# Performance work log

Measured on AMD Instinct MI355X. Metric: run time of the kernel, lower is better.

## Reference

```python
import jax, jax.numpy as jnp
import numpy as np

N_HEAD = 16


def setup_inputs() -> dict:
    key = jax.random.key(0)
    k1, k2, k3 = jax.random.split(key, 3)
    B, T, C = 2, 2048, 1024
    x = jax.random.normal(k1, (B, T, C), dtype=jnp.float32)
    # stored as [in, out] so projection is x @ w (equiv. to torch Linear with W=[out,in])
    w_attn = jax.random.normal(k2, (C, 3 * C), dtype=jnp.float32) * 0.02
    w_proj = jax.random.normal(k3, (C, C), dtype=jnp.float32) * 0.02
    return {"x": x, "w_attn": w_attn, "w_proj": w_proj}


def reference(x, w_attn, w_proj):
    B, T, C = x.shape
    H = N_HEAD
    D = C // H
    qkv = x @ w_attn                                  # [B,T,3C]
    q, k, v = jnp.split(qkv, 3, axis=-1)
    q = q.reshape(B, T, H, D).transpose(0, 2, 1, 3)   # [B,H,T,D]
    k = k.reshape(B, T, H, D).transpose(0, 2, 1, 3)
    v = v.reshape(B, T, H, D).transpose(0, 2, 1, 3)
    scale = 1.0 / jnp.sqrt(jnp.asarray(D, dtype=x.dtype))
    att = jnp.einsum("bhqd,bhkd->bhqk", q, k) * scale  # [B,H,T,T]
    causal = jnp.tril(jnp.ones((T, T), dtype=bool))
    att = jnp.where(causal[None, None], att, jnp.finfo(att.dtype).min)
    att = jax.nn.softmax(att, axis=-1)                 # dropout p=0 (eval)
    y = jnp.einsum("bhqk,bhkd->bhqd", att, v)          # [B,H,T,D]
    y = y.transpose(0, 2, 1, 3).reshape(B, T, C)
    return y @ w_proj
```

## Files before the change

kernel.cpp:

```cpp
#include <hip/hip_runtime.h>

using u16 = unsigned short;
using u32 = unsigned int;

typedef __attribute__((ext_vector_type(8))) short s16x8;
typedef __attribute__((ext_vector_type(4))) short s16x4;
typedef __attribute__((ext_vector_type(8))) __bf16 bf16x8;
typedef __attribute__((ext_vector_type(4))) float f32x4;

static __device__ __forceinline__ u16 f2bf(float f) {
  u32 u = __builtin_bit_cast(u32, f);
  u32 r = u + 0x7FFFu + ((u >> 16) & 1u);
  return (u16)(r >> 16);
}

static __device__ __forceinline__ f32x4 mfma16(s16x8 a, s16x8 b, f32x4 c) {
  return __builtin_amdgcn_mfma_f32_16x16x32_bf16(
      __builtin_bit_cast(bf16x8, a), __builtin_bit_cast(bf16x8, b), c, 0, 0, 0);
}

#define GLOAD_LDS16(gp, lp)                                                    \
  __builtin_amdgcn_global_load_lds(                                            \
      (const __attribute__((address_space(1))) void*)(gp),                     \
      (__attribute__((address_space(3))) void*)(lp), 16, 0, 0)

__global__ __launch_bounds__(256) void k_cvt(const float* __restrict__ in,
                                             u16* __restrict__ out, int n) {
  int i = (blockIdx.x * 256 + threadIdx.x) * 8;
  if (i >= n) return;
  const float4 v0 = *(const float4*)(in + i);
  const float4 v1 = *(const float4*)(in + i + 4);
  s16x8 o;
  o[0] = f2bf(v0.x); o[1] = f2bf(v0.y); o[2] = f2bf(v0.z); o[3] = f2bf(v0.w);
  o[4] = f2bf(v1.x); o[5] = f2bf(v1.y); o[6] = f2bf(v1.z); o[7] = f2bf(v1.w);
  *(s16x8*)(out + i) = o;
}

__global__ __launch_bounds__(256) void k_transpose_cvt(const float* __restrict__ src,
                                                       u16* __restrict__ dst,
                                                       int K, int N) {
  __shared__ float tile[64][65];
  const int n0 = blockIdx.x * 64, k0 = blockIdx.y * 64;
  const int c = threadIdx.x & 63, r4 = threadIdx.x >> 6;
#pragma unroll
  for (int i = 0; i < 16; ++i) {
    int r = (i << 2) + r4;
    tile[r][c] = src[(k0 + r) * N + n0 + c];
  }
  __syncthreads();
#pragma unroll
  for (int i = 0; i < 16; ++i) {
    int r = (i << 2) + r4;
    dst[(n0 + r) * K + k0 + c] = f2bf(tile[c][r]);
  }
}

template <int MODE>
__global__ __launch_bounds__(256) void k_gemm(
    const u16* __restrict__ A, const u16* __restrict__ BT,
    u16* __restrict__ qg, u16* __restrict__ kg, u16* __restrict__ vtg,
    float* __restrict__ cout, int M, int N, int K) {
  __shared__ __align__(16) u16 As[128 * 32];
  __shared__ __align__(16) u16 Bs[128 * 32];
  __shared__ __align__(16) u16 Ct[(MODE == 0) ? (128 * 132) : 8];
  const int t = threadIdx.x;
  const int lane = t & 63;
  const int w = t >> 6, wr = w >> 1, wc = w & 1;
  const int lrow = lane & 15, lkg = lane >> 4;
  const int m0 = blockIdx.y * 128, n0 = blockIdx.x * 128;

  const int ch1 = t + 256;
  const int ra0 = t >> 2, ca0 = (t & 3) << 3;
  const int ra1 = ch1 >> 2, ca1 = (ch1 & 3) << 3;
  const u16* gA0 = A + (m0 + ra0) * K + ca0;
  const u16* gA1 = A + (m0 + ra1) * K + ca1;
  const u16* gB0 = BT + (n0 + ra0) * K + ca0;
  const u16* gB1 = BT + (n0 + ra1) * K + ca1;
  u16* lA0 = &As[t * 8];
  u16* lA1 = &As[ch1 * 8];
  u16* lB0 = &Bs[t * 8];
  u16* lB1 = &Bs[ch1 * 8];

  f32x4 acc[4][4];
#pragma unroll
  for (int m = 0; m < 4; ++m)
#pragma unroll
    for (int n = 0; n < 4; ++n) acc[m][n] = (f32x4){0.f, 0.f, 0.f, 0.f};

  for (int k0 = 0; k0 < K; k0 += 32) {
    GLOAD_LDS16(gA0 + k0, lA0);
    GLOAD_LDS16(gA1 + k0, lA1);
    GLOAD_LDS16(gB0 + k0, lB0);
    GLOAD_LDS16(gB1 + k0, lB1);
    __syncthreads();
    s16x8 af[4], bfr[4];
#pragma unroll
    for (int m = 0; m < 4; ++m)
      af[m] = *(const s16x8*)&As[(wr * 64 + m * 16 + lrow) * 32 + lkg * 8];
#pragma unroll
    for (int n = 0; n < 4; ++n)
      bfr[n] = *(const s16x8*)&Bs[(wc * 64 + n * 16 + lrow) * 32 + lkg * 8];
#pragma unroll
    for (int m = 0; m < 4; ++m)
#pragma unroll
      for (int n = 0; n < 4; ++n) acc[m][n] = mfma16(af[m], bfr[n], acc[m][n]);
    __syncthreads();
  }

  if (MODE == 0) {
    const int part = n0 >> 10;
    const int b = m0 >> 11;
    const int tt0 = m0 & 2047;
    if (part < 2) {
#pragma unroll
      for (int m = 0; m < 4; ++m)
#pragma unroll
        for (int n = 0; n < 4; ++n)
#pragma unroll
          for (int r = 0; r < 4; ++r) {
            const int tl = wr * 64 + m * 16 + lkg * 4 + r;
            const int rem = (n0 & 1023) + wc * 64 + n * 16 + lrow;
            const int h = rem >> 6, d = rem & 63;
            const int bh = b * 16 + h;
            const float v = acc[m][n][r];
            if (part == 0)
              qg[(bh * 2048 + tt0 + tl) * 64 + d] = f2bf(v * 0.18033688f);
            else
              kg[(bh * 2048 + tt0 + tl) * 64 + d] = f2bf(v);
          }
    } else {
#pragma unroll
      for (int m = 0; m < 4; ++m)
#pragma unroll
        for (int n = 0; n < 4; ++n) {
          const int cl2 = wc * 64 + n * 16 + lrow;
          const int tl = wr * 64 + m * 16 + lkg * 4;
          s16x4 pk;
#pragma unroll
          for (int r = 0; r < 4; ++r) pk[r] = f2bf(acc[m][n][r]);
          *(s16x4*)&Ct[cl2 * 132 + tl] = pk;
        }
      __syncthreads();
      const long vrow0 = (long)b * 1024 + (n0 & 1023);
      const int cl = t >> 1;
      const int ch = (t & 1) << 6;
      const u16* csrc = &Ct[cl * 132 + ch];
      u16* vdst = vtg + (vrow0 + cl) * 2048 + tt0 + ch;
#pragma unroll
      for (int j = 0; j < 8; ++j) {
        const s16x4 a4 = *(const s16x4*)&csrc[j * 8];
        const s16x4 b4 = *(const s16x4*)&csrc[j * 8 + 4];
        s16x8 v8;
        v8[0] = a4[0]; v8[1] = a4[1]; v8[2] = a4[2]; v8[3] = a4[3];
        v8[4] = b4[0]; v8[5] = b4[1]; v8[6] = b4[2]; v8[7] = b4[3];
        *(s16x8*)&vdst[j * 8] = v8;
      }
    }
  } else {
#pragma unroll
    for (int m = 0; m < 4; ++m)
#pragma unroll
      for (int n = 0; n < 4; ++n)
#pragma unroll
        for (int r = 0; r < 4; ++r) {
          const int rg = m0 + wr * 64 + m * 16 + lkg * 4 + r;
          const int cg = n0 + wc * 64 + n * 16 + lrow;
          cout[rg * N + cg] = acc[m][n][r];
        }
  }
}

__global__ __launch_bounds__(256) void k_attn(const u16* __restrict__ qg,
                                              const u16* __restrict__ kg,
                                              const u16* __restrict__ vtg,
                                              u16* __restrict__ yb) {
  __shared__ __align__(16) u16 Ks[2][64 * 64];
  __shared__ __align__(16) u16 Vs[2][64 * 64];
  __shared__ __align__(16) u16 Ps[4][32 * 72];
  const int t = threadIdx.x;
  const int lane = t & 63, w = t >> 6;
  const int lrow = lane & 15, lkg = lane >> 4;
  const int bx = blockIdx.x, by = blockIdx.y;
  const int qs = (by & 16) ? (15 - bx) : bx;
  const int bh = by;
  const int qw0 = qs * 128 + w * 32;
  const int hb = bh & 15, bb = bh >> 4;
  const int sw = lrow & 7;
  const f32x4 z4 = {0.f, 0.f, 0.f, 0.f};

  const u16* kbase = kg + ((long)bh << 11) * 64;
  const u16* vbase = vtg + ((long)bh << 6) * 2048;

  const int srow = lane >> 3;
  const int sxor8 = ((lane & 7) ^ srow) << 3;

  s16x8 aq[2][2];
#pragma unroll
  for (int m = 0; m < 2; ++m)
#pragma unroll
    for (int kk = 0; kk < 2; ++kk)
      aq[m][kk] = *(const s16x8*)&qg[((bh << 11) + qw0 + m * 16 + lrow) * 64 +
                                     kk * 32 + lkg * 8];

  f32x4 o[2][4];
  float mst[2], lst[2];
#pragma unroll
  for (int m = 0; m < 2; ++m) {
#pragma unroll
    for (int d = 0; d < 4; ++d) o[m][d] = z4;
    mst[m] = -3e38f;
    lst[m] = 0.f;
  }

  const int nt = 2 * qs + 2;

#define STAGE(BUF, TT)                                                         \
  {                                                                            \
    const int kv0s = (TT) << 6;                                                \
    _Pragma("unroll") for (int i = 0; i < 2; ++i) {                            \
      const int rr = ((i * 4 + w) << 3) + srow;                                \
      const int dst = (((i * 4 + w) << 6) + lane) << 3;                        \
      GLOAD_LDS16(kbase + ((kv0s + rr) << 6) + sxor8, &Ks[BUF][dst]);          \
      GLOAD_LDS16(vbase + ((long)rr << 11) + kv0s + sxor8, &Vs[BUF][dst]);     \
    }                                                                          \
  }

  STAGE(0, 0);
  int buf = 0;
  for (int tt = 0; tt < nt; ++tt) {
    const int kv0 = tt << 6;
    if (tt + 1 < nt) {
      STAGE(buf ^ 1, tt + 1);
      asm volatile("s_waitcnt vmcnt(4)" ::: "memory");
    } else {
      asm volatile("s_waitcnt vmcnt(0)" ::: "memory");
    }
    __builtin_amdgcn_s_barrier();
    __builtin_amdgcn_sched_barrier(0);

    if (kv0 < qw0 + 32) {
      f32x4 s[2][4];
      __builtin_amdgcn_s_setprio(1);
#pragma unroll
      for (int c = 0; c < 4; ++c) {
        const int krow = c * 16 + lrow;
        s16x8 bk0 = *(const s16x8*)&Ks[buf][krow * 64 + ((lkg ^ sw) << 3)];
        s16x8 bk1 = *(const s16x8*)&Ks[buf][krow * 64 + (((4 + lkg) ^ sw) << 3)];
#pragma unroll
        for (int m = 0; m < 2; ++m)
          s[m][c] = mfma16(bk1, aq[m][1], mfma16(bk0, aq[m][0], z4));
      }
      __builtin_amdgcn_s_setprio(0);

      if (kv0 + 64 > qw0) {
#pragma unroll
        for (int m = 0; m < 2; ++m) {
          const int qrow = qw0 + m * 16 + lrow;
#pragma unroll
          for (int c = 0; c < 4; ++c) {
            const int kvb = kv0 + c * 16 + lkg * 4;
#pragma unroll
            for (int r = 0; r < 4; ++r)
              if (kvb + r > qrow) s[m][c][r] = -3e38f;
          }
        }
      }

      u16* PW = Ps[w];
#pragma unroll
      for (int m = 0; m < 2; ++m) {
        float lm = s[m][0][0];
#pragma unroll
        for (int c = 0; c < 4; ++c)
#pragma unroll
          for (int r = 0; r < 4; ++r) lm = fmaxf(lm, s[m][c][r]);
        lm = fmaxf(lm, __shfl_xor(lm, 16));
        lm = fmaxf(lm, __shfl_xor(lm, 32));
        const float mn = fmaxf(mst[m], lm);
        const float alm = exp2f(mst[m] - mn);
        mst[m] = mn;
        float ss = 0.f;
#pragma unroll
        for (int c = 0; c < 4; ++c)
#pragma unroll
          for (int r = 0; r < 4; ++r) {
            const float p = exp2f(s[m][c][r] - mn);
            s[m][c][r] = p;
            ss += p;
          }
        ss += __shfl_xor(ss, 16);
        ss += __shfl_xor(ss, 32);
        lst[m] = alm * lst[m] + ss;
#pragma unroll
        for (int d = 0; d < 4; ++d) o[m][d] *= alm;
#pragma unroll
        for (int c = 0; c < 4; ++c) {
          s16x4 pk;
#pragma unroll
          for (int r = 0; r < 4; ++r) pk[r] = f2bf(s[m][c][r]);
          *(s16x4*)&PW[(m * 16 + lrow) * 72 + c * 16 + lkg * 4] = pk;
        }
      }

      s16x8 pb[2][2];
#pragma unroll
      for (int m = 0; m < 2; ++m)
#pragma unroll
        for (int kk = 0; kk < 2; ++kk)
          pb[m][kk] =
              *(const s16x8*)&PW[(m * 16 + lrow) * 72 + kk * 32 + lkg * 8];

      __builtin_amdgcn_s_setprio(1);
#pragma unroll
      for (int d = 0; d < 4; ++d) {
        const int vrow = d * 16 + lrow;
        s16x8 bv0 = *(const s16x8*)&Vs[buf][vrow * 64 + ((lkg ^ sw) << 3)];
        s16x8 bv1 = *(const s16x8*)&Vs[buf][vrow * 64 + (((4 + lkg) ^ sw) << 3)];
#pragma unroll
        for (int m = 0; m < 2; ++m)
          o[m][d] = mfma16(bv1, pb[m][1], mfma16(bv0, pb[m][0], o[m][d]));
      }
      __builtin_amdgcn_s_setprio(0);
    }

    __builtin_amdgcn_s_barrier();
    buf ^= 1;
  }

#pragma unroll
  for (int m = 0; m < 2; ++m) {
    const float inv = 1.0f / lst[m];
    const int q = qw0 + m * 16 + lrow;
    u16* yrow = yb + ((long)((bb << 11) + q)) * 1024 + hb * 64;
#pragma unroll
    for (int d = 0; d < 4; ++d) {
      s16x4 pk;
#pragma unroll
      for (int r = 0; r < 4; ++r) pk[r] = f2bf(o[m][d][r] * inv);
      *(s16x4*)&yrow[d * 16 + lkg * 4] = pk;
    }
  }
#undef STAGE
}

extern "C" void kernel_launch(void* const* d_in, const int* in_sizes, int n_in,
                              void* d_out, int out_size, void* d_ws,
                              size_t ws_size, hipStream_t stream) {
  const float* x = (const float*)d_in[0];
  const float* wa = (const float*)d_in[1];
  const float* wp = (const float*)d_in[2];
  float* out = (float*)d_out;
  u16* ws = (u16*)d_ws;

  u16* xb = ws;
  u16* wat = xb + 4194304;
  u16* wpt = wat + 3145728;
  u16* qg = wpt + 1048576;
  u16* kg = qg + 4194304;
  u16* vtg = kg + 4194304;
  u16* yb = vtg + 4194304;

  k_cvt<<<2048, 256, 0, stream>>>(x, xb, 4194304);
  k_transpose_cvt<<<dim3(48, 16), 256, 0, stream>>>(wa, wat, 1024, 3072);
  k_transpose_cvt<<<dim3(16, 16), 256, 0, stream>>>(wp, wpt, 1024, 1024);
  k_gemm<0><<<dim3(24, 32), 256, 0, stream>>>(xb, wat, qg, kg, vtg, nullptr,
                                              4096, 3072, 1024);
  k_attn<<<dim3(16, 32), 256, 0, stream>>>(qg, kg, vtg, yb);
  k_gemm<1><<<dim3(8, 32), 256, 0, stream>>>(yb, wpt, nullptr, nullptr, nullptr,
                                             out, 4096, 1024, 1024);
}
```

Before: 224.2 us.

## Compute softmax row sums via MFMA with ones, pack bf16 pairs, add smaller-tile output GEMM

In the attention kernel, the scalar row-sum of probabilities and its cross-lane shuffles are replaced by an MFMA against a ones vector over the bf16 P fragments. Probabilities are now packed with a paired float-to-bf16 intrinsic. The output projection switches to a new GEMM with 64x128 tiles, doubling the block count to improve occupancy on the small N=1024 problem. The new GEMM uses a single LDS buffer with two barriers per K step and no prefetch overlap. The row sum is now taken from bf16-rounded P, which changes numerics slightly.

```diff
diff --git a/kernel.cpp b/kernel.cpp
--- a/kernel.cpp
+++ b/kernel.cpp
@@ -1,4 +1,5 @@
 #include <hip/hip_runtime.h>
+#include <hip/hip_bf16.h>
 
 using u16 = unsigned short;
 using u32 = unsigned int;
@@ -7,11 +8,19 @@
 typedef __attribute__((ext_vector_type(4))) short s16x4;
 typedef __attribute__((ext_vector_type(8))) __bf16 bf16x8;
 typedef __attribute__((ext_vector_type(4))) float f32x4;
+typedef __attribute__((ext_vector_type(2))) unsigned u32x2;
 
 static __device__ __forceinline__ u16 f2bf(float f) {
   u32 u = __builtin_bit_cast(u32, f);
   u32 r = u + 0x7FFFu + ((u >> 16) & 1u);
   return (u16)(r >> 16);
+}
+
+static __device__ __forceinline__ u32 pk2bf(float lo, float hi) {
+  __hip_bfloat162 h = __float22bfloat162_rn(make_float2(lo, hi));
+  u32 r;
+  __builtin_memcpy(&r, &h, 4);
+  return r;
 }
 
 static __device__ __forceinline__ f32x4 mfma16(s16x8 a, s16x8 b, f32x4 c) {
@@ -168,6 +177,63 @@
           cout[rg * N + cg] = acc[m][n][r];
         }
   }
+}
+
+__global__ __launch_bounds__(256) void k_gemm2(const u16* __restrict__ A,
+                                               const u16* __restrict__ BT,
+                                               float* __restrict__ cout, int M,
+                                               int N, int K) {
+  __shared__ __align__(16) u16 As[64 * 32];
+  __shared__ __align__(16) u16 Bs[128 * 32];
+  const int t = threadIdx.x;
+  const int lane = t & 63;
+  const int w = t >> 6, wr = w >> 1, wc = w & 1;
+  const int lrow = lane & 15, lkg = lane >> 4;
+  const int m0 = blockIdx.y * 64, n0 = blockIdx.x * 128;
+
+  const int ra = t >> 2, ca = (t & 3) << 3;
+  const u16* gA = A + (m0 + ra) * K + ca;
+  const u16* gB0 = BT + (n0 + ra) * K + ca;
+  const u16* gB1 = BT + (n0 + 64 + ra) * K + ca;
+  u16* lA = &As[t * 8];
+  u16* lB0 = &Bs[t * 8];
+  u16* lB1 = &Bs[(t + 256) * 8];
+
+  f32x4 acc[2][4];
+#pragma unroll
+  for (int m = 0; m < 2; ++m)
+#pragma unroll
+    for (int n = 0; n < 4; ++n) acc[m][n] = (f32x4){0.f, 0.f, 0.f, 0.f};
+
+  for (int k0 = 0; k0 < K; k0 += 32) {
+    GLOAD_LDS16(gA + k0, lA);
+    GLOAD_LDS16(gB0 + k0, lB0);
+    GLOAD_LDS16(gB1 + k0, lB1);
+    __syncthreads();
+    s16x8 af[2], bfr[4];
+#pragma unroll
+    for (int m = 0; m < 2; ++m)
+      af[m] = *(const s16x8*)&As[(wr * 32 + m * 16 + lrow) * 32 + lkg * 8];
+#pragma unroll
+    for (int n = 0; n < 4; ++n)
+      bfr[n] = *(const s16x8*)&Bs[(wc * 64 + n * 16 + lrow) * 32 + lkg * 8];
+#pragma unroll
+    for (int m = 0; m < 2; ++m)
+#pragma unroll
+      for (int n = 0; n < 4; ++n) acc[m][n] = mfma16(af[m], bfr[n], acc[m][n]);
+    __syncthreads();
+  }
+
+#pragma unroll
+  for (int m = 0; m < 2; ++m)
+#pragma unroll
+    for (int n = 0; n < 4; ++n)
+#pragma unroll
+      for (int r = 0; r < 4; ++r) {
+        const int rg = m0 + wr * 32 + m * 16 + lkg * 4 + r;
+        const int cg = n0 + wc * 64 + n * 16 + lrow;
+        cout[rg * N + cg] = acc[m][n][r];
+      }
 }
 
 __global__ __launch_bounds__(256) void k_attn(const u16* __restrict__ qg,
@@ -187,6 +253,8 @@
   const int hb = bh & 15, bb = bh >> 4;
   const int sw = lrow & 7;
   const f32x4 z4 = {0.f, 0.f, 0.f, 0.f};
+  const s16x8 ones8 = {0x3F80, 0x3F80, 0x3F80, 0x3F80,
+                       0x3F80, 0x3F80, 0x3F80, 0x3F80};
 
   const u16* kbase = kg + ((long)bh << 11) * 64;
   const u16* vbase = vtg + ((long)bh << 6) * 2048;
@@ -203,13 +271,14 @@
                                      kk * 32 + lkg * 8];
 
   f32x4 o[2][4];
-  float mst[2], lst[2];
+  f32x4 os[2];
+  float mst[2];
 #pragma unroll
   for (int m = 0; m < 2; ++m) {
 #pragma unroll
     for (int d = 0; d < 4; ++d) o[m][d] = z4;
+    os[m] = z4;
     mst[m] = -3e38f;
-    lst[m] = 0.f;
   }
 
   const int nt = 2 * qs + 2;
@@ -279,26 +348,18 @@
         const float mn = fmaxf(mst[m], lm);
         const float alm = exp2f(mst[m] - mn);
         mst[m] = mn;
-        float ss = 0.f;
-#pragma unroll
-        for (int c = 0; c < 4; ++c)
-#pragma unroll
-          for (int r = 0; r < 4; ++r) {
-            const float p = exp2f(s[m][c][r] - mn);
-            s[m][c][r] = p;
-            ss += p;
-          }
-        ss += __shfl_xor(ss, 16);
-        ss += __shfl_xor(ss, 32);
-        lst[m] = alm * lst[m] + ss;
 #pragma unroll
         for (int d = 0; d < 4; ++d) o[m][d] *= alm;
+        os[m] *= alm;
 #pragma unroll
         for (int c = 0; c < 4; ++c) {
-          s16x4 pk;
-#pragma unroll
-          for (int r = 0; r < 4; ++r) pk[r] = f2bf(s[m][c][r]);
-          *(s16x4*)&PW[(m * 16 + lrow) * 72 + c * 16 + lkg * 4] = pk;
+          const float p0 = exp2f(s[m][c][0] - mn);
+          const float p1 = exp2f(s[m][c][1] - mn);
+          const float p2 = exp2f(s[m][c][2] - mn);
+          const float p3 = exp2f(s[m][c][3] - mn);
+          const s16x4 pk4 =
+              __builtin_bit_cast(s16x4, (u32x2){pk2bf(p0, p1), pk2bf(p2, p3)});
+          *(s16x4*)&PW[(m * 16 + lrow) * 72 + c * 16 + lkg * 4] = pk4;
         }
       }
 
@@ -320,6 +381,9 @@
         for (int m = 0; m < 2; ++m)
           o[m][d] = mfma16(bv1, pb[m][1], mfma16(bv0, pb[m][0], o[m][d]));
       }
+#pragma unroll
+      for (int m = 0; m < 2; ++m)
+        os[m] = mfma16(ones8, pb[m][1], mfma16(ones8, pb[m][0], os[m]));
       __builtin_amdgcn_s_setprio(0);
     }
 
@@ -329,15 +393,15 @@
 
 #pragma unroll
   for (int m = 0; m < 2; ++m) {
-    const float inv = 1.0f / lst[m];
+    const float inv = 1.0f / os[m][0];
     const int q = qw0 + m * 16 + lrow;
     u16* yrow = yb + ((long)((bb << 11) + q)) * 1024 + hb * 64;
 #pragma unroll
     for (int d = 0; d < 4; ++d) {
-      s16x4 pk;
-#pragma unroll
-      for (int r = 0; r < 4; ++r) pk[r] = f2bf(o[m][d][r] * inv);
-      *(s16x4*)&yrow[d * 16 + lkg * 4] = pk;
+      const s16x4 pk4 = __builtin_bit_cast(
+          s16x4, (u32x2){pk2bf(o[m][d][0] * inv, o[m][d][1] * inv),
+                         pk2bf(o[m][d][2] * inv, o[m][d][3] * inv)});
+      *(s16x4*)&yrow[d * 16 + lkg * 4] = pk4;
     }
   }
 #undef STAGE
@@ -366,6 +430,5 @@
   k_gemm<0><<<dim3(24, 32), 256, 0, stream>>>(xb, wat, qg, kg, vtg, nullptr,
                                               4096, 3072, 1024);
   k_attn<<<dim3(16, 32), 256, 0, stream>>>(qg, kg, vtg, yb);
-  k_gemm<1><<<dim3(8, 32), 256, 0, stream>>>(yb, wpt, nullptr, nullptr, nullptr,
-                                             out, 4096, 1024, 1024);
-}
+  k_gemm2<<<dim3(8, 64), 256, 0, stream>>>(yb, wpt, out, 4096, 1024, 1024);
+}
```

New measurement: 214.8 us. 4.2% less time.
